# Kernel tuning notes

Hardware: AMD Instinct MI355X
Metric: run time of the kernel (lower is better)

## Reference

```python
import jax, jax.numpy as jnp
import numpy as np

H = 2048        # hidden_size
NH = 16         # query heads
NKV = 4         # kv heads (= NH//4, from k_proj shape H x H//4)
HD = H // NH    # head_dim = 128
B, S = 2, 2048
SCALE = 1.0 / (HD ** 0.5)


def _rope(x, cos, sin):
    # x: [B, h, S, d]; cos/sin: [S, d//2]; rotate complex pairs (even, odd)
    xr = x[..., 0::2]
    xi = x[..., 1::2]
    c = cos[None, None, :x.shape[2], :]
    s = sin[None, None, :x.shape[2], :]
    out_r = xr * c - xi * s
    out_i = xr * s + xi * c
    return jnp.stack([out_r, out_i], axis=-1).reshape(x.shape)


def setup_inputs() -> dict:
    key = jax.random.key(0)
    ks = jax.random.split(key, 6)
    hidden_states = jax.random.normal(ks[0], (B, S, H), dtype=jnp.float32)
    # RoPE table (theta = 10000), head_dim//2 frequencies
    inv_freq = 1.0 / (10000.0 ** (np.arange(0, HD, 2, dtype=np.float32) / HD))
    angles = np.arange(S, dtype=np.float32)[:, None] * inv_freq[None, :]
    freqs_cos = jnp.asarray(np.cos(angles), dtype=jnp.float32)
    freqs_sin = jnp.asarray(np.sin(angles), dtype=jnp.float32)
    w = 0.02  # keep activations in a sane range
    Wq = jax.random.normal(ks[1], (H, H), dtype=jnp.float32) * w
    Wk = jax.random.normal(ks[2], (H // 4, H), dtype=jnp.float32) * w
    Wv = jax.random.normal(ks[3], (H // 4, H), dtype=jnp.float32) * w
    Wo = jax.random.normal(ks[4], (H, H), dtype=jnp.float32) * w
    return {"hidden_states": hidden_states, "freqs_cos": freqs_cos,
            "freqs_sin": freqs_sin, "Wq": Wq, "Wk": Wk, "Wv": Wv, "Wo": Wo}


def reference(hidden_states, freqs_cos, freqs_sin, Wq, Wk, Wv, Wo):
    b, s, _ = hidden_states.shape
    q = hidden_states @ Wq.T                      # [B,S,H]
    k = hidden_states @ Wk.T                      # [B,S,H/4]
    v = hidden_states @ Wv.T                      # [B,S,H/4]
    q = q.reshape(b, s, NH, HD).transpose(0, 2, 1, 3)    # [B,NH,S,HD]
    k = k.reshape(b, s, NKV, HD).transpose(0, 2, 1, 3)   # [B,NKV,S,HD]
    v = v.reshape(b, s, NKV, HD).transpose(0, 2, 1, 3)
    q = _rope(q, freqs_cos, freqs_sin)
    k = _rope(k, freqs_cos, freqs_sin)
    # GQA: each kv head serves NH//NKV query heads
    k_rep = jnp.repeat(k, NH // NKV, axis=1)      # [B,NH,S,HD]
    v_rep = jnp.repeat(v, NH // NKV, axis=1)
    scores = jnp.einsum('bhqd,bhkd->bhqk', q, k_rep) * SCALE  # [B,NH,S,S]
    probs = jax.nn.softmax(scores, axis=-1)
    out = jnp.einsum('bhqk,bhkd->bhqd', probs, v_rep)         # [B,NH,S,HD]
    out = out.transpose(0, 2, 1, 3).reshape(b, s, H)
    return out @ Wo.T
```

## Files before the change

kernel.cpp:

```cpp
#include <hip/hip_runtime.h>

typedef __bf16 bf16_t;
typedef bf16_t bf16x8 __attribute__((ext_vector_type(8)));
typedef bf16_t bf16x4 __attribute__((ext_vector_type(4)));
typedef bf16_t bf16x2 __attribute__((ext_vector_type(2)));
typedef float f32x4 __attribute__((ext_vector_type(4)));
typedef float f32x16 __attribute__((ext_vector_type(16)));
typedef unsigned int u32x4 __attribute__((ext_vector_type(4)));

typedef const __attribute__((address_space(1))) void* as1_cvp;
typedef __attribute__((address_space(3))) void* as3_vp;

__device__ __forceinline__ void gload16(const void* g, void* l) {
  __builtin_amdgcn_global_load_lds((as1_cvp)g, (as3_vp)l, 16, 0, 0);
}

__device__ __forceinline__ unsigned pxor32(unsigned x) {
  return (unsigned)__shfl_xor((int)x, 32);
}

__global__ __launch_bounds__(256) void cvt_kernel(const float* __restrict__ src,
                                                  bf16_t* __restrict__ dst, int n8) {
  int i = blockIdx.x * 256 + threadIdx.x;
  if (i >= n8) return;
  int idx = i * 8;
  float4 a = *(const float4*)(src + idx);
  float4 b = *(const float4*)(src + idx + 4);
  bf16x8 o;
  o[0] = (bf16_t)a.x; o[1] = (bf16_t)a.y; o[2] = (bf16_t)a.z; o[3] = (bf16_t)a.w;
  o[4] = (bf16_t)b.x; o[5] = (bf16_t)b.y; o[6] = (bf16_t)b.z; o[7] = (bf16_t)b.w;
  *(bf16x8*)(dst + idx) = o;
}

#define BM 128
#define BN 128
#define BK 64

__global__ __launch_bounds__(256, 2) void gemm_bt(const bf16_t* __restrict__ A,
                                                  const bf16_t* __restrict__ B,
                                                  float* __restrict__ C,
                                                  int M, int N, int K) {
  __shared__ alignas(16) bf16_t As[BM * BK];
  __shared__ alignas(16) bf16_t Bs[BN * BK];
  const int t = threadIdx.x;
  const int lane = t & 63, w = t >> 6;
  const int wm = w >> 1, wn = w & 1;
  const int lr = lane & 15, lg = lane >> 4;
  const int m0 = blockIdx.y * BM, n0 = blockIdx.x * BN;
  const int srow = t >> 3, scol = (t & 7) * 8;

  f32x4 acc[4][4] = {};

  for (int kb = 0; kb < K; kb += BK) {
    __syncthreads();
#pragma unroll
    for (int i = 0; i < 4; ++i) {
      gload16(A + (size_t)(m0 + srow + 32 * i) * K + kb + scol, As + i * 2048 + t * 8);
      gload16(B + (size_t)(n0 + srow + 32 * i) * K + kb + scol, Bs + i * 2048 + t * 8);
    }
    __syncthreads();
#pragma unroll
    for (int kk = 0; kk < 2; ++kk) {
      const int ko = kk * 32 + lg * 8;
      bf16x8 af[4], bfr[4];
#pragma unroll
      for (int r = 0; r < 4; ++r)
        af[r] = *(const bf16x8*)(As + (wm * 64 + r * 16 + lr) * BK + ko);
#pragma unroll
      for (int c = 0; c < 4; ++c)
        bfr[c] = *(const bf16x8*)(Bs + (wn * 64 + c * 16 + lr) * BK + ko);
#pragma unroll
      for (int r = 0; r < 4; ++r)
#pragma unroll
        for (int c = 0; c < 4; ++c)
          acc[r][c] = __builtin_amdgcn_mfma_f32_16x16x32_bf16(af[r], bfr[c], acc[r][c], 0, 0, 0);
    }
  }
#pragma unroll
  for (int r = 0; r < 4; ++r)
#pragma unroll
    for (int c = 0; c < 4; ++c)
#pragma unroll
      for (int b = 0; b < 4; ++b)
        C[(size_t)(m0 + wm * 64 + r * 16 + lg * 4 + b) * N + n0 + wn * 64 + c * 16 + lr] =
            acc[r][c][b];
}

__global__ __launch_bounds__(256, 2) void gemm_qkv(const bf16_t* __restrict__ A,
                                                   const bf16_t* __restrict__ B,
                                                   const float* __restrict__ cs,
                                                   const float* __restrict__ sn,
                                                   bf16_t* __restrict__ qr,
                                                   bf16_t* __restrict__ kr,
                                                   bf16_t* __restrict__ vt) {
  __shared__ alignas(16) bf16_t As[BM * BK];
  __shared__ alignas(16) bf16_t Bs[BN * BK];
  const int K = 2048;
  const int t = threadIdx.x;
  const int lane = t & 63, w = t >> 6;
  const int wm = w >> 1, wn = w & 1;
  const int lr = lane & 15, lg = lane >> 4;
  const int m0 = blockIdx.y * BM, n0 = blockIdx.x * BN;
  const int srow = t >> 3, scol = (t & 7) * 8;

  f32x4 acc[4][4] = {};

  for (int kb = 0; kb < K; kb += BK) {
    __syncthreads();
#pragma unroll
    for (int i = 0; i < 4; ++i) {
      gload16(A + (size_t)(m0 + srow + 32 * i) * K + kb + scol, As + i * 2048 + t * 8);
      gload16(B + (size_t)(n0 + srow + 32 * i) * K + kb + scol, Bs + i * 2048 + t * 8);
    }
    __syncthreads();
#pragma unroll
    for (int kk = 0; kk < 2; ++kk) {
      const int ko = kk * 32 + lg * 8;
      bf16x8 af[4], bfr[4];
#pragma unroll
      for (int r = 0; r < 4; ++r)
        af[r] = *(const bf16x8*)(As + (wm * 64 + r * 16 + lr) * BK + ko);
#pragma unroll
      for (int c = 0; c < 4; ++c)
        bfr[c] = *(const bf16x8*)(Bs + (wn * 64 + c * 16 + lr) * BK + ko);
#pragma unroll
      for (int r = 0; r < 4; ++r)
#pragma unroll
        for (int c = 0; c < 4; ++c)
          acc[r][c] = __builtin_amdgcn_mfma_f32_16x16x32_bf16(af[r], bfr[c], acc[r][c], 0, 0, 0);
    }
  }

  const int head = n0 >> 7;
  const int bb2 = m0 >> 11;
  const int sbase = (m0 & 2047) + wm * 64 + lg * 4;
  if (head < 20) {
    bf16_t* dst = (head < 16) ? qr + (size_t)(bb2 * 16 + head) * 2048 * 128
                              : kr + (size_t)(bb2 * 4 + (head - 16)) * 2048 * 128;
    const bool evn = (lr & 1) == 0;
#pragma unroll
    for (int r = 0; r < 4; ++r)
#pragma unroll
      for (int c = 0; c < 4; ++c) {
        const int cw = wn * 64 + c * 16 + lr;
        const int dix = cw >> 1;
#pragma unroll
        for (int b = 0; b < 4; ++b) {
          const int s = sbase + r * 16 + b;
          float own = acc[r][c][b];
          float prt = __shfl_xor(own, 1);
          if (evn) {
            float cc = cs[s * 64 + dix];
            float ssn = sn[s * 64 + dix];
            bf16x2 pr;
            pr[0] = (bf16_t)(own * cc - prt * ssn);
            pr[1] = (bf16_t)(own * ssn + prt * cc);
            *(bf16x2*)(dst + (size_t)s * 128 + cw) = pr;
          }
        }
      }
  } else {
    bf16_t* dst = vt + (size_t)(bb2 * 4 + (head - 20)) * 128 * 2048;
#pragma unroll
    for (int r = 0; r < 4; ++r)
#pragma unroll
      for (int c = 0; c < 4; ++c) {
        const int cw = wn * 64 + c * 16 + lr;
        const int s = sbase + r * 16;
        bf16x4 v4;
#pragma unroll
        for (int b = 0; b < 4; ++b) v4[b] = (bf16_t)acc[r][c][b];
        *(bf16x4*)(dst + (size_t)cw * 2048 + s) = v4;
      }
  }
}

#define KVB 64
__global__ __launch_bounds__(256, 2) void attn_kernel(const bf16_t* __restrict__ Q,
                                                      const bf16_t* __restrict__ Kg,
                                                      const bf16_t* __restrict__ Vg,
                                                      bf16_t* __restrict__ O) {
  __shared__ alignas(16) bf16_t Ks[2][16 * KVB * 8];
  __shared__ alignas(16) bf16_t Vs[2][8 * 128 * 8];
  const int t = threadIdx.x;
  const int lane = t & 63, w = t >> 6;
  const int l31 = lane & 31, hi = lane >> 5;
  const int bid = ((blockIdx.x & 7) << 6) | (blockIdx.x >> 3);
  const int qt = bid & 15;
  const int h = (bid >> 4) & 15;
  const int bb = bid >> 8;
  const int kvh = h >> 2;

  const bf16_t* Qh = Q + (((size_t)bb * 16 + h) * 2048 + qt * 128 + w * 32) * 128;
  const bf16_t* Kh = Kg + ((size_t)bb * 4 + kvh) * 2048 * 128;
  const bf16_t* Vh = Vg + ((size_t)bb * 4 + kvh) * 128 * 2048;

  bf16x8 qf[8];
#pragma unroll
  for (int c = 0; c < 8; ++c)
    qf[c] = *(const bf16x8*)(Qh + l31 * 128 + c * 16 + hi * 8);

  f32x16 o[4] = {};
  float m2 = -1e30f;
  float ls = 0.f;
  const float sm = 0.08838834764831845f * 1.44269504088896f;

#define STAGE_K(buf, kb)                                                                \
  _Pragma("unroll") for (int i = 0; i < 4; ++i)                                         \
    gload16(Kh + (size_t)((kb) + (t & 63)) * 128 + (i * 4 + (t >> 6)) * 8,              \
            &Ks[buf][(i * 256 + t) * 8]);
#define STAGE_V(buf, kb)                                                                \
  _Pragma("unroll") for (int i = 0; i < 4; ++i)                                         \
    gload16(Vh + (size_t)(t & 127) * 2048 + (kb) + (i * 2 + (t >> 7)) * 8,              \
            &Vs[buf][(i * 256 + t) * 8]);

  STAGE_K(0, 0);
  STAGE_V(0, 0);
  __syncthreads();

  for (int tt = 0; tt < 32; ++tt) {
    const int cur = tt & 1;
    if (tt < 31) {
      STAGE_K(cur ^ 1, (tt + 1) * KVB);
      STAGE_V(cur ^ 1, (tt + 1) * KVB);
    }
    const bf16_t* Kc = Ks[cur];
    const bf16_t* Vc = Vs[cur];

    f32x16 s0 = {}, s1 = {};
    __builtin_amdgcn_s_setprio(1);
#pragma unroll
    for (int c = 0; c < 8; ++c) {
      bf16x8 kf0 = *(const bf16x8*)(Kc + ((c * 2 + hi) * 64 + l31) * 8);
      bf16x8 kf1 = *(const bf16x8*)(Kc + ((c * 2 + hi) * 64 + 32 + l31) * 8);
      s0 = __builtin_amdgcn_mfma_f32_32x32x16_bf16(kf0, qf[c], s0, 0, 0, 0);
      s1 = __builtin_amdgcn_mfma_f32_32x32x16_bf16(kf1, qf[c], s1, 0, 0, 0);
    }
    __builtin_amdgcn_s_setprio(0);

    float tm[8];
#pragma unroll
    for (int j = 0; j < 8; ++j)
      tm[j] = fmaxf(fmaxf(s0[2 * j], s0[2 * j + 1]), fmaxf(s1[2 * j], s1[2 * j + 1]));
    float mxr = fmaxf(fmaxf(fmaxf(tm[0], tm[1]), fmaxf(tm[2], tm[3])),
                      fmaxf(fmaxf(tm[4], tm[5]), fmaxf(tm[6], tm[7])));
    mxr = fmaxf(mxr, __shfl_xor(mxr, 32));
    float mx = mxr * sm;

    if (__any(mx > m2 + 8.0f)) {
      float mn = fmaxf(m2, mx);
      float resc = exp2f(m2 - mn);
      m2 = mn;
      ls *= resc;
      float rf[16];
#pragma unroll
      for (int r = 0; r < 16; ++r) rf[r] = __shfl(resc, (r & 3) + 8 * (r >> 2) + 4 * hi);
#pragma unroll
      for (int dblk = 0; dblk < 4; ++dblk)
#pragma unroll
        for (int r = 0; r < 16; ++r) o[dblk][r] *= rf[r];
    }
#pragma unroll
    for (int r = 0; r < 16; ++r) {
      float p0 = exp2f(fmaf(s0[r], sm, -m2));
      float p1 = exp2f(fmaf(s1[r], sm, -m2));
      s0[r] = p0; s1[r] = p1;
      ls += p0 + p1;
    }

    unsigned Wa[8], Wb[8];
#pragma unroll
    for (int s = 0; s < 8; ++s) {
      bf16x2 a = {(bf16_t)s0[2 * s], (bf16_t)s0[2 * s + 1]};
      bf16x2 b = {(bf16_t)s1[2 * s], (bf16_t)s1[2 * s + 1]};
      Wa[s] = __builtin_bit_cast(unsigned, a);
      Wb[s] = __builtin_bit_cast(unsigned, b);
    }
    bf16x8 pf[4];
    {
      unsigned wv[16];
#pragma unroll
      for (int g = 0; g < 4; ++g) {
        unsigned* W = (g & 2) ? Wb : Wa;
        const int o4 = (g & 1) * 4;
        unsigned pp0 = pxor32(W[o4 + 0]);
        unsigned pp1 = pxor32(W[o4 + 1]);
        unsigned pp2 = pxor32(W[o4 + 2]);
        unsigned pp3 = pxor32(W[o4 + 3]);
        wv[g * 4 + 0] = hi ? pp2 : W[o4 + 0];
        wv[g * 4 + 1] = hi ? pp3 : W[o4 + 1];
        wv[g * 4 + 2] = hi ? W[o4 + 2] : pp0;
        wv[g * 4 + 3] = hi ? W[o4 + 3] : pp1;
      }
      u32x4 pw0 = {wv[0], wv[1], wv[2], wv[3]};
      u32x4 pw1 = {wv[4], wv[5], wv[6], wv[7]};
      u32x4 pw2 = {wv[8], wv[9], wv[10], wv[11]};
      u32x4 pw3 = {wv[12], wv[13], wv[14], wv[15]};
      pf[0] = __builtin_bit_cast(bf16x8, pw0);
      pf[1] = __builtin_bit_cast(bf16x8, pw1);
      pf[2] = __builtin_bit_cast(bf16x8, pw2);
      pf[3] = __builtin_bit_cast(bf16x8, pw3);
    }

    __builtin_amdgcn_s_setprio(1);
#pragma unroll
    for (int kk = 0; kk < 4; ++kk) {
#pragma unroll
      for (int dblk = 0; dblk < 4; ++dblk) {
        bf16x8 vf = *(const bf16x8*)(Vc + ((kk * 2 + hi) * 128 + dblk * 32 + l31) * 8);
        o[dblk] = __builtin_amdgcn_mfma_f32_32x32x16_bf16(pf[kk], vf, o[dblk], 0, 0, 0);
      }
    }
    __builtin_amdgcn_s_setprio(0);
    __syncthreads();
  }

  float lt = ls + __shfl_xor(ls, 32);
  float rinv = 1.0f / lt;
  float rq[16];
#pragma unroll
  for (int r = 0; r < 16; ++r) rq[r] = __shfl(rinv, (r & 3) + 8 * (r >> 2) + 4 * hi);
  const size_t q0 = (size_t)bb * 2048 + qt * 128 + w * 32;
#pragma unroll
  for (int dblk = 0; dblk < 4; ++dblk)
#pragma unroll
    for (int r = 0; r < 16; ++r) {
      const int qrow = (r & 3) + 8 * (r >> 2) + 4 * hi;
      O[(q0 + qrow) * 2048 + h * 128 + dblk * 32 + l31] = (bf16_t)(o[dblk][r] * rq[r]);
    }
}

extern "C" void kernel_launch(void* const* d_in, const int* in_sizes, int n_in,
                              void* d_out, int out_size, void* d_ws, size_t ws_size,
                              hipStream_t stream) {
  const float* hs = (const float*)d_in[0];
  const float* fc = (const float*)d_in[1];
  const float* fs = (const float*)d_in[2];
  const float* Wq = (const float*)d_in[3];
  const float* Wk = (const float*)d_in[4];
  const float* Wv = (const float*)d_in[5];
  const float* Wo = (const float*)d_in[6];
  float* out = (float*)d_out;

  char* ws = (char*)d_ws;
  bf16_t* hs_b = (bf16_t*)ws;
  bf16_t* wcat = (bf16_t*)(ws + 16777216);
  bf16_t* wo_b = (bf16_t*)(ws + 29360128);
  bf16_t* qr = (bf16_t*)(ws + 37748736);
  bf16_t* kr = (bf16_t*)(ws + 54525952);
  bf16_t* vt = (bf16_t*)(ws + 58720256);
  bf16_t* ao = (bf16_t*)(ws + 62914560);

  cvt_kernel<<<8388608 / 8 / 256, 256, 0, stream>>>(hs, hs_b, 8388608 / 8);
  cvt_kernel<<<4194304 / 8 / 256, 256, 0, stream>>>(Wq, wcat, 4194304 / 8);
  cvt_kernel<<<1048576 / 8 / 256, 256, 0, stream>>>(Wk, wcat + 4194304, 1048576 / 8);
  cvt_kernel<<<1048576 / 8 / 256, 256, 0, stream>>>(Wv, wcat + 5242880, 1048576 / 8);
  cvt_kernel<<<4194304 / 8 / 256, 256, 0, stream>>>(Wo, wo_b, 4194304 / 8);

  dim3 g1(3072 / BN, 4096 / BM);
  gemm_qkv<<<g1, 256, 0, stream>>>(hs_b, wcat, fc, fs, qr, kr, vt);

  attn_kernel<<<512, 256, 0, stream>>>(qr, kr, vt, ao);

  dim3 g2(2048 / BN, 4096 / BM);
  gemm_bt<<<g2, 256, 0, stream>>>(ao, wo_b, out, 4096, 2048, 2048);
}
```

Before: 247.4 us.

## Software-pipeline attention: overlap next tile's QK^T with current softmax and PV

Restructures the attention main loop so the QK^T MFMAs for tile t+1 are issued before the softmax, packing and PV MFMAs of tile t. V staging moves to a triple buffer to keep the lagging V tile alive while the next ones are prefetched. The aim is to let matrix-core work overlap the exp/shuffle-heavy softmax phase. In exchange it holds an extra pair of 32x32 score accumulators in registers and uses more LDS, which may pressure occupancy at 2 blocks per CU.

```diff
diff --git a/kernel.cpp b/kernel.cpp
--- a/kernel.cpp
+++ b/kernel.cpp
@@ -176,12 +176,81 @@
 }
 
 #define KVB 64
+
+#define SOFTMAX_PACK_PV(S0, S1, VSLOT)                                                   \
+  {                                                                                      \
+    float tm[8];                                                                         \
+    _Pragma("unroll") for (int j = 0; j < 8; ++j)                                        \
+        tm[j] = fmaxf(fmaxf(S0[2 * j], S0[2 * j + 1]), fmaxf(S1[2 * j], S1[2 * j + 1])); \
+    float mxr = fmaxf(fmaxf(fmaxf(tm[0], tm[1]), fmaxf(tm[2], tm[3])),                   \
+                      fmaxf(fmaxf(tm[4], tm[5]), fmaxf(tm[6], tm[7])));                  \
+    mxr = fmaxf(mxr, __shfl_xor(mxr, 32));                                               \
+    float mx = mxr * sm;                                                                 \
+    if (__any(mx > m2 + 8.0f)) {                                                         \
+      float mn = fmaxf(m2, mx);                                                          \
+      float resc = exp2f(m2 - mn);                                                       \
+      m2 = mn;                                                                           \
+      ls *= resc;                                                                        \
+      float rf[16];                                                                      \
+      _Pragma("unroll") for (int r = 0; r < 16; ++r)                                     \
+          rf[r] = __shfl(resc, (r & 3) + 8 * (r >> 2) + 4 * hi);                         \
+      _Pragma("unroll") for (int dblk = 0; dblk < 4; ++dblk)                             \
+          _Pragma("unroll") for (int r = 0; r < 16; ++r) o[dblk][r] *= rf[r];            \
+    }                                                                                    \
+    _Pragma("unroll") for (int r = 0; r < 16; ++r) {                                     \
+      float p0 = exp2f(fmaf(S0[r], sm, -m2));                                            \
+      float p1 = exp2f(fmaf(S1[r], sm, -m2));                                            \
+      S0[r] = p0; S1[r] = p1;                                                            \
+      ls += p0 + p1;                                                                     \
+    }                                                                                    \
+    unsigned Wa[8], Wb[8];                                                               \
+    _Pragma("unroll") for (int s = 0; s < 8; ++s) {                                      \
+      bf16x2 a = {(bf16_t)S0[2 * s], (bf16_t)S0[2 * s + 1]};                             \
+      bf16x2 b = {(bf16_t)S1[2 * s], (bf16_t)S1[2 * s + 1]};                             \
+      Wa[s] = __builtin_bit_cast(unsigned, a);                                           \
+      Wb[s] = __builtin_bit_cast(unsigned, b);                                           \
+    }                                                                                    \
+    bf16x8 pf[4];                                                                        \
+    {                                                                                    \
+      unsigned wv[16];                                                                   \
+      _Pragma("unroll") for (int g = 0; g < 4; ++g) {                                    \
+        unsigned* W = (g & 2) ? Wb : Wa;                                                 \
+        const int o4 = (g & 1) * 4;                                                      \
+        unsigned pp0 = pxor32(W[o4 + 0]);                                                \
+        unsigned pp1 = pxor32(W[o4 + 1]);                                                \
+        unsigned pp2 = pxor32(W[o4 + 2]);                                                \
+        unsigned pp3 = pxor32(W[o4 + 3]);                                                \
+        wv[g * 4 + 0] = hi ? pp2 : W[o4 + 0];                                            \
+        wv[g * 4 + 1] = hi ? pp3 : W[o4 + 1];                                            \
+        wv[g * 4 + 2] = hi ? W[o4 + 2] : pp0;                                            \
+        wv[g * 4 + 3] = hi ? W[o4 + 3] : pp1;                                            \
+      }                                                                                  \
+      u32x4 pw0 = {wv[0], wv[1], wv[2], wv[3]};                                          \
+      u32x4 pw1 = {wv[4], wv[5], wv[6], wv[7]};                                          \
+      u32x4 pw2 = {wv[8], wv[9], wv[10], wv[11]};                                        \
+      u32x4 pw3 = {wv[12], wv[13], wv[14], wv[15]};                                      \
+      pf[0] = __builtin_bit_cast(bf16x8, pw0);                                           \
+      pf[1] = __builtin_bit_cast(bf16x8, pw1);                                           \
+      pf[2] = __builtin_bit_cast(bf16x8, pw2);                                           \
+      pf[3] = __builtin_bit_cast(bf16x8, pw3);                                           \
+    }                                                                                    \
+    const bf16_t* Vp = Vs[VSLOT];                                                        \
+    __builtin_amdgcn_s_setprio(1);                                                       \
+    _Pragma("unroll") for (int kk = 0; kk < 4; ++kk) {                                   \
+      _Pragma("unroll") for (int dblk = 0; dblk < 4; ++dblk) {                           \
+        bf16x8 vf = *(const bf16x8*)(Vp + ((kk * 2 + hi) * 128 + dblk * 32 + l31) * 8);  \
+        o[dblk] = __builtin_amdgcn_mfma_f32_32x32x16_bf16(pf[kk], vf, o[dblk], 0, 0, 0); \
+      }                                                                                  \
+    }                                                                                    \
+    __builtin_amdgcn_s_setprio(0);                                                       \
+  }
+
 __global__ __launch_bounds__(256, 2) void attn_kernel(const bf16_t* __restrict__ Q,
                                                       const bf16_t* __restrict__ Kg,
                                                       const bf16_t* __restrict__ Vg,
                                                       bf16_t* __restrict__ O) {
   __shared__ alignas(16) bf16_t Ks[2][16 * KVB * 8];
-  __shared__ alignas(16) bf16_t Vs[2][8 * 128 * 8];
+  __shared__ alignas(16) bf16_t Vs[3][8 * 128 * 8];
   const int t = threadIdx.x;
   const int lane = t & 63, w = t >> 6;
   const int l31 = lane & 31, hi = lane >> 5;
@@ -214,106 +283,44 @@
     gload16(Vh + (size_t)(t & 127) * 2048 + (kb) + (i * 2 + (t >> 7)) * 8,              \
             &Vs[buf][(i * 256 + t) * 8]);
 
+#define QKT(DST0, DST1, KBUF)                                                           \
+  {                                                                                     \
+    const bf16_t* Kc = Ks[KBUF];                                                        \
+    __builtin_amdgcn_s_setprio(1);                                                      \
+    _Pragma("unroll") for (int c = 0; c < 8; ++c) {                                     \
+      bf16x8 kf0 = *(const bf16x8*)(Kc + ((c * 2 + hi) * 64 + l31) * 8);                \
+      bf16x8 kf1 = *(const bf16x8*)(Kc + ((c * 2 + hi) * 64 + 32 + l31) * 8);           \
+      DST0 = __builtin_amdgcn_mfma_f32_32x32x16_bf16(kf0, qf[c], DST0, 0, 0, 0);        \
+      DST1 = __builtin_amdgcn_mfma_f32_32x32x16_bf16(kf1, qf[c], DST1, 0, 0, 0);        \
+    }                                                                                   \
+    __builtin_amdgcn_s_setprio(0);                                                      \
+  }
+
   STAGE_K(0, 0);
   STAGE_V(0, 0);
   __syncthreads();
-
-  for (int tt = 0; tt < 32; ++tt) {
-    const int cur = tt & 1;
+  STAGE_K(1, KVB);
+  STAGE_V(1, KVB);
+  f32x16 sp0 = {}, sp1 = {};
+  QKT(sp0, sp1, 0);
+  __syncthreads();
+
+  int vstage = 2;
+  int vread = 0;
+  for (int tt = 1; tt < 32; ++tt) {
     if (tt < 31) {
-      STAGE_K(cur ^ 1, (tt + 1) * KVB);
-      STAGE_V(cur ^ 1, (tt + 1) * KVB);
-    }
-    const bf16_t* Kc = Ks[cur];
-    const bf16_t* Vc = Vs[cur];
-
-    f32x16 s0 = {}, s1 = {};
-    __builtin_amdgcn_s_setprio(1);
-#pragma unroll
-    for (int c = 0; c < 8; ++c) {
-      bf16x8 kf0 = *(const bf16x8*)(Kc + ((c * 2 + hi) * 64 + l31) * 8);
-      bf16x8 kf1 = *(const bf16x8*)(Kc + ((c * 2 + hi) * 64 + 32 + l31) * 8);
-      s0 = __builtin_amdgcn_mfma_f32_32x32x16_bf16(kf0, qf[c], s0, 0, 0, 0);
-      s1 = __builtin_amdgcn_mfma_f32_32x32x16_bf16(kf1, qf[c], s1, 0, 0, 0);
-    }
-    __builtin_amdgcn_s_setprio(0);
-
-    float tm[8];
-#pragma unroll
-    for (int j = 0; j < 8; ++j)
-      tm[j] = fmaxf(fmaxf(s0[2 * j], s0[2 * j + 1]), fmaxf(s1[2 * j], s1[2 * j + 1]));
-    float mxr = fmaxf(fmaxf(fmaxf(tm[0], tm[1]), fmaxf(tm[2], tm[3])),
-                      fmaxf(fmaxf(tm[4], tm[5]), fmaxf(tm[6], tm[7])));
-    mxr = fmaxf(mxr, __shfl_xor(mxr, 32));
-    float mx = mxr * sm;
-
-    if (__any(mx > m2 + 8.0f)) {
-      float mn = fmaxf(m2, mx);
-      float resc = exp2f(m2 - mn);
-      m2 = mn;
-      ls *= resc;
-      float rf[16];
-#pragma unroll
-      for (int r = 0; r < 16; ++r) rf[r] = __shfl(resc, (r & 3) + 8 * (r >> 2) + 4 * hi);
-#pragma unroll
-      for (int dblk = 0; dblk < 4; ++dblk)
-#pragma unroll
-        for (int r = 0; r < 16; ++r) o[dblk][r] *= rf[r];
-    }
-#pragma unroll
-    for (int r = 0; r < 16; ++r) {
-      float p0 = exp2f(fmaf(s0[r], sm, -m2));
-      float p1 = exp2f(fmaf(s1[r], sm, -m2));
-      s0[r] = p0; s1[r] = p1;
-      ls += p0 + p1;
-    }
-
-    unsigned Wa[8], Wb[8];
-#pragma unroll
-    for (int s = 0; s < 8; ++s) {
-      bf16x2 a = {(bf16_t)s0[2 * s], (bf16_t)s0[2 * s + 1]};
-      bf16x2 b = {(bf16_t)s1[2 * s], (bf16_t)s1[2 * s + 1]};
-      Wa[s] = __builtin_bit_cast(unsigned, a);
-      Wb[s] = __builtin_bit_cast(unsigned, b);
-    }
-    bf16x8 pf[4];
-    {
-      unsigned wv[16];
-#pragma unroll
-      for (int g = 0; g < 4; ++g) {
-        unsigned* W = (g & 2) ? Wb : Wa;
-        const int o4 = (g & 1) * 4;
-        unsigned pp0 = pxor32(W[o4 + 0]);
-        unsigned pp1 = pxor32(W[o4 + 1]);
-        unsigned pp2 = pxor32(W[o4 + 2]);
-        unsigned pp3 = pxor32(W[o4 + 3]);
-        wv[g * 4 + 0] = hi ? pp2 : W[o4 + 0];
-        wv[g * 4 + 1] = hi ? pp3 : W[o4 + 1];
-        wv[g * 4 + 2] = hi ? W[o4 + 2] : pp0;
-        wv[g * 4 + 3] = hi ? W[o4 + 3] : pp1;
-      }
-      u32x4 pw0 = {wv[0], wv[1], wv[2], wv[3]};
-      u32x4 pw1 = {wv[4], wv[5], wv[6], wv[7]};
-      u32x4 pw2 = {wv[8], wv[9], wv[10], wv[11]};
-      u32x4 pw3 = {wv[12], wv[13], wv[14], wv[15]};
-      pf[0] = __builtin_bit_cast(bf16x8, pw0);
-      pf[1] = __builtin_bit_cast(bf16x8, pw1);
-      pf[2] = __builtin_bit_cast(bf16x8, pw2);
-      pf[3] = __builtin_bit_cast(bf16x8, pw3);
-    }
-
-    __builtin_amdgcn_s_setprio(1);
-#pragma unroll
-    for (int kk = 0; kk < 4; ++kk) {
-#pragma unroll
-      for (int dblk = 0; dblk < 4; ++dblk) {
-        bf16x8 vf = *(const bf16x8*)(Vc + ((kk * 2 + hi) * 128 + dblk * 32 + l31) * 8);
-        o[dblk] = __builtin_amdgcn_mfma_f32_32x32x16_bf16(pf[kk], vf, o[dblk], 0, 0, 0);
-      }
-    }
-    __builtin_amdgcn_s_setprio(0);
-    __syncthreads();
-  }
+      STAGE_K((tt + 1) & 1, (tt + 1) * KVB);
+      STAGE_V(vstage, (tt + 1) * KVB);
+    }
+    f32x16 sc0 = {}, sc1 = {};
+    QKT(sc0, sc1, tt & 1);
+    SOFTMAX_PACK_PV(sp0, sp1, vread);
+    sp0 = sc0; sp1 = sc1;
+    vstage = (vstage == 2) ? 0 : vstage + 1;
+    vread = (vread == 2) ? 0 : vread + 1;
+    __syncthreads();
+  }
+  SOFTMAX_PACK_PV(sp0, sp1, vread);
 
   float lt = ls + __shfl_xor(ls, 32);
   float rinv = 1.0f / lt;
```

Result: slower. 252.8 us (+2.2%).
